# Optimization experiments

Measured on AMD Instinct MI355X. Metric: run time of the kernel, lower is better.

## Reference

```python
import jax, jax.numpy as jnp
import numpy as np
from jax import lax

H, W = 496, 432
NUM_CLASSES = 3
NUM_ROT = 2
A_PER_LOC = NUM_CLASSES * NUM_ROT  # 6
BOX = 7
NMS_PRE = 4096
MAX_NUM = 500
SCORE_THR = 0.1
NMS_THR = 0.5
PI = float(np.pi)


def _make_priors():
    # Anchor3DRangeGenerator equivalent: grid of BEV centers x (3 sizes x 2 rotations)
    xs = jnp.linspace(0.0, 69.12, W, dtype=jnp.float32)
    ys = jnp.linspace(-39.68, 39.68, H, dtype=jnp.float32)
    cy, cx = jnp.meshgrid(ys, xs, indexing='ij')  # [H,W]
    sizes = jnp.array([[3.9, 1.6, 1.56], [0.8, 0.6, 1.73], [1.76, 0.6, 1.73]], jnp.float32)
    szs = jnp.repeat(sizes, NUM_ROT, axis=0)                       # [6,3]
    rots = jnp.tile(jnp.array([0.0, 1.57], jnp.float32), NUM_CLASSES)  # [6]
    cx = jnp.broadcast_to(cx[:, :, None], (H, W, A_PER_LOC))
    cy = jnp.broadcast_to(cy[:, :, None], (H, W, A_PER_LOC))
    cz = jnp.full((H, W, A_PER_LOC), -1.78, jnp.float32)
    wlh = jnp.broadcast_to(szs[None, None], (H, W, A_PER_LOC, 3))
    r = jnp.broadcast_to(rots[None, None], (H, W, A_PER_LOC))
    pri = jnp.concatenate([cx[..., None], cy[..., None], cz[..., None], wlh, r[..., None]], -1)
    return pri.reshape(-1, BOX)  # [H*W*6, 7]


def setup_inputs() -> dict:
    key = jax.random.key(0)
    k1, k2, k3 = jax.random.split(key, 3)
    cls_score = jax.random.normal(k1, (A_PER_LOC * NUM_CLASSES, H, W), jnp.float32)
    bbox_pred = 0.1 * jax.random.normal(k2, (A_PER_LOC * BOX, H, W), jnp.float32)
    dir_cls_pred = jax.random.normal(k3, (A_PER_LOC * 2, H, W), jnp.float32)
    priors = _make_priors()
    return {"cls_score": cls_score, "bbox_pred": bbox_pred,
            "dir_cls_pred": dir_cls_pred, "priors": priors}


def _decode(anchors, deltas):
    xa, ya, za, wa, la, ha, ra = [anchors[:, i] for i in range(7)]
    xt, yt, zt, wt, lt, ht, rt = [deltas[:, i] for i in range(7)]
    za = za + ha / 2
    diag = jnp.sqrt(la ** 2 + wa ** 2)
    xg = xt * diag + xa
    yg = yt * diag + ya
    zg = zt * ha + za
    lg = jnp.exp(lt) * la
    wg = jnp.exp(wt) * wa
    hg = jnp.exp(ht) * ha
    rg = rt + ra
    zg = zg - hg / 2
    return jnp.stack([xg, yg, zg, wg, lg, hg, rg], axis=-1)


def _nms_keep(boxes_xyxy, scores_c, valid_c):
    # Greedy NMS with py_cpu_nms math (+1 pixel convention), fixed-shape masked version.
    n = boxes_xyxy.shape[0]
    order = jnp.argsort(-scores_c)
    b = boxes_xyxy[order]
    v = valid_c[order]
    x1, y1, x2, y2 = b[:, 0], b[:, 1], b[:, 2], b[:, 3]
    areas = (x2 - x1 + 1.0) * (y2 - y1 + 1.0)
    xx1 = jnp.maximum(x1[:, None], x1[None, :])
    yy1 = jnp.maximum(y1[:, None], y1[None, :])
    xx2 = jnp.minimum(x2[:, None], x2[None, :])
    yy2 = jnp.minimum(y2[:, None], y2[None, :])
    inter = jnp.maximum(0.0, xx2 - xx1 + 1.0) * jnp.maximum(0.0, yy2 - yy1 + 1.0)
    iou = inter / (areas[:, None] + areas[None, :] - inter)  # [N,N]
    idx = jnp.arange(n)

    def body(i, keep):
        row = (iou[i] > NMS_THR) & (idx > i)
        return jnp.where(keep[i], keep & ~row, keep)

    keep_sorted = lax.fori_loop(0, n, body, v)
    return jnp.zeros(n, bool).at[order].set(keep_sorted)


def reference(cls_score, bbox_pred, dir_cls_pred, priors):
    # flatten feature maps -> per-anchor predictions
    scores_all = jax.nn.sigmoid(cls_score.transpose(1, 2, 0).reshape(-1, NUM_CLASSES))  # [A,C]
    dir_all = jnp.argmax(dir_cls_pred.transpose(1, 2, 0).reshape(-1, 2), axis=-1)       # [A]
    bp_all = bbox_pred.transpose(1, 2, 0).reshape(-1, BOX)                               # [A,7]
    # nms_pre top-k by best class score
    max_scores = scores_all.max(axis=1)
    _, topk = lax.top_k(max_scores, NMS_PRE)
    pri = priors[topk]
    bp = bp_all[topk]
    sc = scores_all[topk]           # [N,C]
    dsc = dir_all[topk]             # [N]
    bboxes = _decode(pri, bp)       # [N,7] x,y,z,w,l,h,r
    # BEV box -> axis-aligned xyxy (stands in for open3d obb2aabb + xywhr2xyxyr)
    x, y, w, l = bboxes[:, 0], bboxes[:, 1], bboxes[:, 3], bboxes[:, 4]
    boxes_xyxy = jnp.stack([x - w / 2, y - l / 2, x + w / 2, y + l / 2], axis=-1)
    # per-class greedy NMS on the same candidate pool
    valid = sc > SCORE_THR          # [N,C]
    keep = jax.vmap(lambda s, v: _nms_keep(boxes_xyxy, s, v), in_axes=(1, 1))(sc, valid)  # [C,N]
    # merge classes, keep top max_num by score (fixed-shape, padded)
    comb = jnp.where(keep, sc.T, -jnp.inf)                # [C,N]
    top_scores, flat_idx = lax.top_k(comb.reshape(-1), MAX_NUM)
    labels = flat_idx // NMS_PRE
    bidx = flat_idx % NMS_PRE
    sel_b = bboxes[bidx]                                   # [MAX_NUM,7]
    sel_d = dsc[bidx].astype(sel_b.dtype)
    # direction-aware yaw fix (replicates original expression incl. precedence)
    r = sel_b[:, 6]
    dir_rot = r + PI / 2 - jnp.floor(r + 0.5) * PI
    sel_b = sel_b.at[:, 6].set(dir_rot - PI / 2 + PI * sel_d)
    valid_out = jnp.isfinite(top_scores)
    sel_b = jnp.where(valid_out[:, None], sel_b, 0.0)
    out_scores = jnp.where(valid_out, top_scores, 0.0)
    labels = jnp.where(valid_out, labels, -1)
    return sel_b, out_scores, labels
```

## Files before the change

### kernel.cpp

```cpp
#include <hip/hip_runtime.h>
#include <stdint.h>
#include <stddef.h>

constexpr int kH = 496, kW = 432;
constexpr int HWSZ = kH * kW;
constexpr int NANCH = HWSZ * 6;
constexpr int NPRE = 4096;
constexpr int MAXNUM = 500;
constexpr int CAND_CAP = 8192;
constexpr float SCORE_THR_F = 0.1f;
constexpr float PIF  = 3.14159265358979323846f;
constexpr float HPIF = 1.57079632679489661923f;

constexpr int NBINS  = 32768;
constexpr int NPAIR  = NBINS / 2;
constexpr int NB_H   = 256;

constexpr uint64_t PADKEY = 0xFFFFFFFF00000000ull;

constexpr size_t HIST_OFF  = 0;
constexpr size_t MISC_OFF  = 131072;
constexpr size_t ZERO_BYTES= 131072 + 256;
constexpr size_t MS_OFF    = 131328;
constexpr size_t CAND_OFF  = MS_OFF + 4ull * NANCH;
constexpr size_t SEL_OFF   = CAND_OFF + 8ull * CAND_CAP;
constexpr size_t SC3_OFF   = SEL_OFF + 4ull * NPRE;
constexpr size_t DSC_OFF   = SC3_OFF + 4ull * NPRE * 3;
constexpr size_t BB7_OFF   = DSC_OFF + 4ull * NPRE;
constexpr size_t BOX4_OFF  = BB7_OFF + 4ull * NPRE * 7;
constexpr size_t AREA_OFF  = BOX4_OFF + 4ull * NPRE * 4;
constexpr size_t ORD_OFF   = AREA_OFF + 4ull * NPRE;
constexpr size_t VW_OFF    = ORD_OFF + 4ull * 3 * NPRE;
constexpr size_t PMASK_OFF = VW_OFF + 8ull * 3 * 64;
constexpr size_t KEEPW_OFF = PMASK_OFF + 8ull * 3 * NPRE * 64;
constexpr size_t OUTK_OFF  = KEEPW_OFF + 8ull * 3 * 64;

__device__ __forceinline__ float sigmoidf_(float x) { return 1.0f / (1.0f + expf(-x)); }

__device__ __forceinline__ uint64_t readlane64(uint64_t v, int lane) {
  uint32_t lo = (uint32_t)__builtin_amdgcn_readlane((int)(uint32_t)(v & 0xffffffffull), lane);
  uint32_t hi = (uint32_t)__builtin_amdgcn_readlane((int)(uint32_t)(v >> 32), lane);
  return (((uint64_t)hi) << 32) | (uint64_t)lo;
}


__global__ __launch_bounds__(256) void k_score(const float* __restrict__ cls,
                                               float* __restrict__ ms,
                                               uint32_t* __restrict__ hist) {
  __shared__ uint32_t h[NPAIR];
  const int t = threadIdx.x, blk = blockIdx.x;
  for (int i = t; i < NPAIR; i += 256) h[i] = 0;
  __syncthreads();
  for (int p = blk * 256 + t; p < HWSZ; p += NB_H * 256) {
#pragma unroll
    for (int k = 0; k < 6; ++k) {
      float s0 = sigmoidf_(cls[(k * 3 + 0) * HWSZ + p]);
      float s1 = sigmoidf_(cls[(k * 3 + 1) * HWSZ + p]);
      float s2 = sigmoidf_(cls[(k * 3 + 2) * HWSZ + p]);
      float m = fmaxf(s0, fmaxf(s1, s2));
      ms[p * 6 + k] = m;
      uint32_t bin = __float_as_uint(m) >> 15;
      atomicAdd(&h[bin >> 1], 1u << ((bin & 1) * 16));
    }
  }
  __syncthreads();
  for (int i = t; i < NPAIR; i += 256) {
    uint32_t v = h[i];
    if (v) {
      uint32_t lo = v & 0xFFFFu, hi = v >> 16;
      if (lo) atomicAdd(&hist[2 * i],     lo);
      if (hi) atomicAdd(&hist[2 * i + 1], hi);
    }
  }
}

__global__ void k_scanhist(const uint32_t* __restrict__ hist, uint32_t* __restrict__ misc) {
  __shared__ uint32_t part[256];
  __shared__ uint32_t suf[257];
  int t = threadIdx.x;
  int base = t * 128;
  uint32_t s = 0;
  for (int b = 0; b < 128; ++b) s += hist[base + b];
  part[t] = s;
  __syncthreads();
  if (t == 0) {
    uint32_t acc = 0;
    suf[256] = 0;
    for (int q = 255; q >= 0; --q) { suf[q] = acc + part[q]; acc = suf[q]; }
  }
  __syncthreads();
  uint32_t above = suf[t + 1];
  if (above < (uint32_t)NPRE && above + part[t] >= (uint32_t)NPRE) {
    uint32_t acc = above;
    for (int b = base + 127; b >= base; --b) {
      uint32_t h = hist[b];
      if (acc + h >= (uint32_t)NPRE) { misc[1] = (uint32_t)b; misc[2] = acc; break; }
      acc += h;
    }
  }
}

__global__ __launch_bounds__(256) void k_compact(const float* __restrict__ ms,
                                                 uint32_t* __restrict__ misc,
                                                 uint64_t* __restrict__ cand) {
  constexpr int APB = 4096;
  __shared__ uint64_t lbuf[APB];
  __shared__ uint32_t lcnt, lbase;
  const int t = threadIdx.x;
  const int base = blockIdx.x * APB;
  if (t == 0) lcnt = 0;
  __syncthreads();
  const uint32_t B = misc[1];
#pragma unroll
  for (int q = 0; q < 16; ++q) {
    int a = base + q * 256 + t;
    if (a < NANCH) {
      uint32_t bits = __float_as_uint(ms[a]);
      if ((bits >> 15) >= B) {
        uint32_t s = atomicAdd(&lcnt, 1u);
        lbuf[s] = (((uint64_t)(~bits)) << 32) | (uint32_t)a;
      }
    }
  }
  __syncthreads();
  const uint32_t n = lcnt;
  if (t == 0 && n > 0) lbase = atomicAdd(&misc[0], n);
  __syncthreads();
  if (n > 0) {
    const uint32_t b0 = lbase;
    for (uint32_t i = t; i < n; i += 256) {
      uint32_t slot = b0 + i;
      if (slot < (uint32_t)CAND_CAP) cand[slot] = lbuf[i];
    }
  }
}

__global__ __launch_bounds__(256) void k_rank(const uint64_t* __restrict__ cand,
                                              const uint32_t* __restrict__ misc,
                                              uint32_t* __restrict__ sel) {
  const int tid = threadIdx.x, ln = tid & 63;
  const int wave = blockIdx.x * 4 + (tid >> 6);
  const int base = wave * 16;
  uint32_t cnt = misc[0];
  if (cnt > (uint32_t)CAND_CAP) cnt = CAND_CAP;
  uint64_t kr[16];
#pragma unroll
  for (int r = 0; r < 16; ++r) kr[r] = cand[base + r];
  uint32_t rnk[16];
#pragma unroll
  for (int r = 0; r < 16; ++r) rnk[r] = 0;
  const int nch = ((int)cnt + 63) >> 6;
  for (int ch = 0; ch < nch; ++ch) {
    uint64_t ck = cand[ch * 64 + ln];
    uint64_t vm = __ballot(ch * 64 + ln < (int)cnt);
#pragma unroll
    for (int r = 0; r < 16; ++r)
      rnk[r] += (uint32_t)__popcll(__ballot(ck < kr[r]) & vm);
  }
#pragma unroll
  for (int r = 0; r < 16; ++r) {
    int row = base + r;
    if (ln == 0 && row < (int)cnt && rnk[r] < (uint32_t)NPRE)
      sel[rnk[r]] = (uint32_t)kr[r];
  }
}

__global__ void k_gather(const uint32_t* __restrict__ sel, const float* __restrict__ cls,
                         const float* __restrict__ bbp, const float* __restrict__ dirp,
                         const float* __restrict__ priors, float* __restrict__ sc3,
                         uint32_t* __restrict__ dsc, float* __restrict__ bb7,
                         float* __restrict__ box4, float* __restrict__ areaA) {
  int i = blockIdx.x * 256 + threadIdx.x;
  if (i >= NPRE) return;
  uint32_t a = sel[i];
  uint32_t p = a / 6u;
  uint32_t k = a - p * 6u;
#pragma unroll
  for (int c = 0; c < 3; ++c) sc3[i * 3 + c] = sigmoidf_(cls[(k * 3 + c) * HWSZ + p]);
  float d0 = dirp[(k * 2 + 0) * HWSZ + p];
  float d1 = dirp[(k * 2 + 1) * HWSZ + p];
  dsc[i] = (d1 > d0) ? 1u : 0u;
  float dt[7], pr[7];
#pragma unroll
  for (int q = 0; q < 7; ++q) dt[q] = bbp[(k * 7 + q) * HWSZ + p];
#pragma unroll
  for (int q = 0; q < 7; ++q) pr[q] = priors[(size_t)a * 7 + q];
  float za = pr[2] + pr[5] * 0.5f;
  float diag = sqrtf(pr[4] * pr[4] + pr[3] * pr[3]);
  float xg = dt[0] * diag + pr[0];
  float yg = dt[1] * diag + pr[1];
  float zg = dt[2] * pr[5] + za;
  float wg = expf(dt[3]) * pr[3];
  float lg = expf(dt[4]) * pr[4];
  float hg = expf(dt[5]) * pr[5];
  float rg = dt[6] + pr[6];
  zg = zg - hg * 0.5f;
  bb7[i * 7 + 0] = xg; bb7[i * 7 + 1] = yg; bb7[i * 7 + 2] = zg;
  bb7[i * 7 + 3] = wg; bb7[i * 7 + 4] = lg; bb7[i * 7 + 5] = hg; bb7[i * 7 + 6] = rg;
  float x1 = xg - wg * 0.5f, y1 = yg - lg * 0.5f;
  float x2 = xg + wg * 0.5f, y2 = yg + lg * 0.5f;
  box4[i * 4 + 0] = x1; box4[i * 4 + 1] = y1; box4[i * 4 + 2] = x2; box4[i * 4 + 3] = y2;
  areaA[i] = (x2 - x1 + 1.0f) * (y2 - y1 + 1.0f);
}

__global__ __launch_bounds__(256) void k_rankcls(const float* __restrict__ sc3,
                                                 uint32_t* __restrict__ ord) {
  const int tid = threadIdx.x, ln = tid & 63;
  const int c = blockIdx.y;
  const int wave = blockIdx.x * 4 + (tid >> 6);
  const int base = wave * 16;
  uint64_t kr[16];
#pragma unroll
  for (int r = 0; r < 16; ++r) {
    int j = base + r;
    kr[r] = (((uint64_t)(~__float_as_uint(sc3[j * 3 + c]))) << 32) | (uint32_t)j;
  }
  uint32_t rnk[16];
#pragma unroll
  for (int r = 0; r < 16; ++r) rnk[r] = 0;
  for (int ch = 0; ch < NPRE / 64; ++ch) {
    int j = ch * 64 + ln;
    uint64_t ck = (((uint64_t)(~__float_as_uint(sc3[j * 3 + c]))) << 32) | (uint32_t)j;
#pragma unroll
    for (int r = 0; r < 16; ++r)
      rnk[r] += (uint32_t)__popcll(__ballot(ck < kr[r]));
  }
#pragma unroll
  for (int r = 0; r < 16; ++r)
    if (ln == 0) ord[c * NPRE + rnk[r]] = (uint32_t)(base + r);
}

__global__ __launch_bounds__(1024) void k_vwords(const uint32_t* __restrict__ ord,
                                                 const float* __restrict__ sc3,
                                                 uint64_t* __restrict__ vwords) {
  int c = blockIdx.x, t = threadIdx.x, ln = t & 63;
  for (int k = 0; k < 4; ++k) {
    int i = k * 1024 + t;
    uint32_t pos = ord[c * NPRE + i];
    uint64_t m = __ballot(sc3[pos * 3 + c] > SCORE_THR_F);
    if (ln == 0) vwords[c * 64 + (i >> 6)] = m;
  }
}

__global__ void k_mask(const uint32_t* __restrict__ ord, const float* __restrict__ box4,
                       const float* __restrict__ areaA, uint64_t* __restrict__ pmask) {
  int c = blockIdx.z, it = blockIdx.y, jt = blockIdx.x, t = threadIdx.x;
  if (jt < it) return;
  __shared__ float jx1[64], jy1[64], jx2[64], jy2[64], jar[64];
  int j = ord[c * NPRE + jt * 64 + t];
  jx1[t] = box4[j * 4 + 0]; jy1[t] = box4[j * 4 + 1];
  jx2[t] = box4[j * 4 + 2]; jy2[t] = box4[j * 4 + 3];
  jar[t] = areaA[j];
  __syncthreads();
  int I = it * 64 + t;
  int i = ord[c * NPRE + I];
  float x1 = box4[i * 4 + 0], y1 = box4[i * 4 + 1];
  float x2 = box4[i * 4 + 2], y2 = box4[i * 4 + 3];
  float ar = areaA[i];
  uint64_t bits = 0;
  for (int b = 0; b < 64; ++b) {
    float xx1 = fmaxf(x1, jx1[b]), yy1 = fmaxf(y1, jy1[b]);
    float xx2 = fminf(x2, jx2[b]), yy2 = fminf(y2, jy2[b]);
    float iw = fmaxf(0.0f, xx2 - xx1 + 1.0f);
    float ih = fmaxf(0.0f, yy2 - yy1 + 1.0f);
    float inter = iw * ih;
    float iou = inter / (ar + jar[b] - inter);
    bits |= ((uint64_t)(iou > 0.5f)) << b;
  }
  pmask[((size_t)(c * NPRE + I)) * 64 + (size_t)jt] = bits;
}

__global__ __launch_bounds__(320) void k_nms(const uint64_t* __restrict__ pmask,
                                             const uint64_t* __restrict__ vwords,
                                             uint64_t* __restrict__ keepw) {
  __shared__ uint64_t tile[2][64 * 64];
  __shared__ int s_stop[2];
  const int c = blockIdx.x;
  const int tid = threadIdx.x;
  const int wv = tid >> 6;
  const int ln = tid & 63;
  const uint64_t* pm = pmask + (size_t)c * NPRE * 64;

  if (tid == 0) { s_stop[0] = 0; s_stop[1] = 0; }
  if (wv > 0) {
    int l = tid - 64;
    const ulonglong2* src2 = (const ulonglong2*)pm;
    ulonglong2* dst2 = (ulonglong2*)tile[0];
#pragma unroll
    for (int q = 0; q < 8; ++q) dst2[q * 256 + l] = src2[q * 256 + l];
  }
  __syncthreads();

  uint64_t avail = 0, keepbits = 0;
  int cnt = 0;
  if (wv == 0) avail = vwords[c * 64 + ln];

  for (int T = 0; T < 64; ++T) {
    const int cb = T & 1;
    if (wv > 0) {
      if (T + 1 < 64) {
        int l = tid - 64;
        const ulonglong2* src2 = (const ulonglong2*)(pm + (size_t)(T + 1) * 64 * 64);
        ulonglong2* dst2 = (ulonglong2*)tile[cb ^ 1];
#pragma unroll
        for (int q = 0; q < 8; ++q) dst2[q * 256 + l] = src2[q * 256 + l];
      }
    } else {
      const uint64_t* tp = tile[cb];
      uint64_t awT = readlane64(avail, T);
      uint64_t pf[8];
#pragma unroll
      for (int u = 0; u < 8; ++u) pf[u] = tp[u * 64 + ln];
      uint64_t kwT = 0;
#pragma unroll
      for (int r = 0; r < 64; ++r) {
        uint64_t cur = pf[r & 7];
        if (r + 8 < 64) pf[r & 7] = tp[(r + 8) * 64 + ln];
        bool kp = ((awT >> r) & 1ull) != 0ull;
        if (kp) {
          avail &= ~cur;
          awT &= ~readlane64(cur, T);
          kwT |= (1ull << r);
        }
      }
      if (ln == T) keepbits = kwT;
      cnt += (int)__popcll(kwT);
      if (ln == 0 && cnt >= MAXNUM) s_stop[cb] = 1;
    }
    __syncthreads();
    if (s_stop[cb]) break;
  }
  if (wv == 0) keepw[c * 64 + ln] = keepbits;
}

__global__ __launch_bounds__(1024) void k_collect(const uint64_t* __restrict__ keepw,
                                                  const uint32_t* __restrict__ ord,
                                                  const float* __restrict__ sc3,
                                                  uint64_t* __restrict__ outk,
                                                  uint32_t* __restrict__ misc) {
  const int c = blockIdx.x, t = threadIdx.x, w = t >> 6, ln = t & 63;
  if (c == 3) {
    int i = 3 * MAXNUM + t;
    if (i < 2048) outk[i] = PADKEY;
    return;
  }
  __shared__ uint32_t wsum[16];
  uint32_t bits4 = 0;
#pragma unroll
  for (int q = 0; q < 4; ++q) {
    int i = t * 4 + q;
    uint32_t b = (uint32_t)((keepw[c * 64 + (i >> 6)] >> (i & 63)) & 1ull);
    bits4 |= b << q;
  }
  uint32_t cnt = __popc(bits4);
  uint32_t incl = cnt;
#pragma unroll
  for (int d = 1; d < 64; d <<= 1) { uint32_t u = __shfl_up(incl, d, 64); if (ln >= d) incl += u; }
  if (ln == 63) wsum[w] = incl;
  __syncthreads();
  uint32_t wb = 0, total = 0;
#pragma unroll
  for (int i = 0; i < 16; ++i) { uint32_t v = wsum[i]; total += v; if (i < w) wb += v; }
  uint32_t r = wb + incl - cnt;
#pragma unroll
  for (int q = 0; q < 4; ++q) {
    if ((bits4 >> q) & 1u) {
      if (r < (uint32_t)MAXNUM) {
        uint32_t pos = ord[c * NPRE + t * 4 + q];
        uint32_t sb = __float_as_uint(sc3[pos * 3 + c]);
        outk[c * MAXNUM + r] = (((uint64_t)(~sb)) << 32) | (uint32_t)(c * NPRE + pos);
      }
      ++r;
    }
  }
  uint32_t Vc = total < (uint32_t)MAXNUM ? total : (uint32_t)MAXNUM;
  if (t == 0) misc[8 + c] = Vc;
  for (uint32_t s = Vc + t; s < (uint32_t)MAXNUM; s += 1024)
    outk[c * MAXNUM + s] = PADKEY;
}

__global__ __launch_bounds__(256) void k_emit(const uint64_t* __restrict__ outk,
                                              const uint32_t* __restrict__ misc,
                                              const float* __restrict__ bb7,
                                              const uint32_t* __restrict__ dsc,
                                              float* __restrict__ out) {
  const int tid = threadIdx.x, ln = tid & 63;
  const int wave = blockIdx.x * 4 + (tid >> 6);
  const int base = wave * 16;
  uint64_t kr[16];
#pragma unroll
  for (int r = 0; r < 16; ++r) kr[r] = outk[base + r];
  uint32_t rnk[16];
#pragma unroll
  for (int r = 0; r < 16; ++r) rnk[r] = 0;
  for (int ch = 0; ch < 2048 / 64; ++ch) {
    uint64_t ck = outk[ch * 64 + ln];
#pragma unroll
    for (int r = 0; r < 16; ++r)
      rnk[r] += (uint32_t)__popcll(__ballot(ck < kr[r]));
  }
  if (ln == 0) {
#pragma unroll
    for (int r = 0; r < 16; ++r) {
      uint64_t key = kr[r];
      uint32_t rk = rnk[r];
      if (key != PADKEY && rk < (uint32_t)MAXNUM) {
        uint32_t flat = (uint32_t)key;
        float score = __uint_as_float(~((uint32_t)(key >> 32)));
        int cc = (int)(flat >> 12);
        int pos = (int)(flat & 4095u);
        const float* b = bb7 + (size_t)pos * 7;
        float rr0 = b[6];
        float dir_rot = rr0 + HPIF - floorf(rr0 + 0.5f) * PIF;
        float rr = dir_rot - HPIF + PIF * (float)dsc[pos];
#pragma unroll
        for (int q = 0; q < 6; ++q) out[rk * 7 + q] = b[q];
        out[rk * 7 + 6] = rr;
        out[7 * MAXNUM + rk] = score;
        out[8 * MAXNUM + rk] = (float)cc;
      }
    }
  }
  if (blockIdx.x == 0) {
    uint32_t V = misc[8] + misc[9] + misc[10];
    for (uint32_t s = V + tid; s < (uint32_t)MAXNUM; s += 256) {
#pragma unroll
      for (int q = 0; q < 7; ++q) out[s * 7 + q] = 0.0f;
      out[7 * MAXNUM + s] = 0.0f;
      out[8 * MAXNUM + s] = -1.0f;
    }
  }
}

extern "C" void kernel_launch(void* const* d_in, const int* in_sizes, int n_in,
                              void* d_out, int out_size, void* d_ws, size_t ws_size,
                              hipStream_t stream) {
  (void)in_sizes; (void)n_in; (void)out_size; (void)ws_size;
  const float* cls    = (const float*)d_in[0];
  const float* bbp    = (const float*)d_in[1];
  const float* dirp   = (const float*)d_in[2];
  const float* priors = (const float*)d_in[3];
  char* ws = (char*)d_ws;

  uint32_t* hist   = (uint32_t*)(ws + HIST_OFF);
  uint32_t* misc   = (uint32_t*)(ws + MISC_OFF);
  float*    ms     = (float*)(ws + MS_OFF);
  uint64_t* cand   = (uint64_t*)(ws + CAND_OFF);
  uint32_t* sel    = (uint32_t*)(ws + SEL_OFF);
  float*    sc3    = (float*)(ws + SC3_OFF);
  uint32_t* dsc    = (uint32_t*)(ws + DSC_OFF);
  float*    bb7    = (float*)(ws + BB7_OFF);
  float*    box4   = (float*)(ws + BOX4_OFF);
  float*    areaA  = (float*)(ws + AREA_OFF);
  uint32_t* ord    = (uint32_t*)(ws + ORD_OFF);
  uint64_t* vwords = (uint64_t*)(ws + VW_OFF);
  uint64_t* pmask  = (uint64_t*)(ws + PMASK_OFF);
  uint64_t* keepw  = (uint64_t*)(ws + KEEPW_OFF);
  uint64_t* outk   = (uint64_t*)(ws + OUTK_OFF);

  hipMemsetAsync(ws, 0, ZERO_BYTES, stream);
  k_score<<<NB_H, 256, 0, stream>>>(cls, ms, hist);
  k_scanhist<<<1, 256, 0, stream>>>(hist, misc);
  k_compact<<<(NANCH + 4095) / 4096, 256, 0, stream>>>(ms, misc, cand);
  k_rank<<<CAND_CAP / (4 * 16), 256, 0, stream>>>(cand, misc, sel);
  k_gather<<<NPRE / 256, 256, 0, stream>>>(sel, cls, bbp, dirp, priors, sc3, dsc, bb7, box4, areaA);
  k_rankcls<<<dim3(NPRE / (4 * 16), 3), 256, 0, stream>>>(sc3, ord);
  k_vwords<<<3, 1024, 0, stream>>>(ord, sc3, vwords);
  k_mask<<<dim3(64, 64, 3), 64, 0, stream>>>(ord, box4, areaA, pmask);
  k_nms<<<3, 320, 0, stream>>>(pmask, vwords, keepw);
  k_collect<<<4, 1024, 0, stream>>>(keepw, ord, sc3, outk, misc);
  k_emit<<<2048 / (4 * 16), 256, 0, stream>>>(outk, misc, bb7, dsc, (float*)d_out);
}
```

Before: 292.1 us.

## Fold histogram scan into compact and vwords into NMS, make NMS sparse

Removes the single-block histogram scan kernel by having every compact block redundantly scan the histogram with a parallel suffix sum to find the threshold bin. Removes the vwords kernel by computing validity ballots inside the NMS kernel. Rewrites NMS as a single wavefront that iterates only over kept boxes per tile, using ctz loops and direct global reads of diagonal and suppression rows instead of double-buffered shared tiles. This saves launches and serial work, but adds redundant histogram reads in each compact block (about 128 KB per block) and latency-bound global loads in NMS.

```diff
diff --git a/kernel.cpp b/kernel.cpp
--- a/kernel.cpp
+++ b/kernel.cpp
@@ -74,51 +74,59 @@
   }
 }
 
-__global__ void k_scanhist(const uint32_t* __restrict__ hist, uint32_t* __restrict__ misc) {
-  __shared__ uint32_t part[256];
-  __shared__ uint32_t suf[257];
-  int t = threadIdx.x;
-  int base = t * 128;
-  uint32_t s = 0;
-  for (int b = 0; b < 128; ++b) s += hist[base + b];
-  part[t] = s;
-  __syncthreads();
-  if (t == 0) {
-    uint32_t acc = 0;
-    suf[256] = 0;
-    for (int q = 255; q >= 0; --q) { suf[q] = acc + part[q]; acc = suf[q]; }
-  }
-  __syncthreads();
-  uint32_t above = suf[t + 1];
-  if (above < (uint32_t)NPRE && above + part[t] >= (uint32_t)NPRE) {
-    uint32_t acc = above;
-    for (int b = base + 127; b >= base; --b) {
-      uint32_t h = hist[b];
-      if (acc + h >= (uint32_t)NPRE) { misc[1] = (uint32_t)b; misc[2] = acc; break; }
-      acc += h;
-    }
-  }
-}
-
 __global__ __launch_bounds__(256) void k_compact(const float* __restrict__ ms,
+                                                 const uint32_t* __restrict__ hist,
                                                  uint32_t* __restrict__ misc,
                                                  uint64_t* __restrict__ cand) {
   constexpr int APB = 4096;
   __shared__ uint64_t lbuf[APB];
-  __shared__ uint32_t lcnt, lbase;
+  __shared__ uint32_t suf[256];
+  __shared__ uint32_t win[256];
+  __shared__ uint32_t lcnt, lbase, sWin, sAbove, sB;
   const int t = threadIdx.x;
   const int base = blockIdx.x * APB;
-  if (t == 0) lcnt = 0;
-  __syncthreads();
-  const uint32_t B = misc[1];
+
+  uint32_t s = 0;
+  const int hbase = t * 128;
+#pragma unroll 16
+  for (int i = 0; i < 128; ++i) s += hist[hbase + i];
+  suf[t] = s;
+  if (t == 0) { lcnt = 0; sB = 0; }
+  __syncthreads();
+  for (int d = 1; d < 256; d <<= 1) {
+    uint32_t v = suf[t] + ((t + d < 256) ? suf[t + d] : 0u);
+    __syncthreads();
+    suf[t] = v;
+    __syncthreads();
+  }
+  {
+    uint32_t sin = suf[t];
+    uint32_t sup = (t < 255) ? suf[t + 1] : 0u;
+    if (sin >= (uint32_t)NPRE && sup < (uint32_t)NPRE) { sWin = (uint32_t)t; sAbove = sup; }
+  }
+  __syncthreads();
+  const uint32_t wbase = sWin * 128u;
+  win[t] = (t < 128) ? hist[wbase + (uint32_t)t] : 0u;
+  __syncthreads();
+  for (int d = 1; d < 256; d <<= 1) {
+    uint32_t v = win[t] + ((t + d < 256) ? win[t + d] : 0u);
+    __syncthreads();
+    win[t] = v;
+    __syncthreads();
+  }
+  if (t < 128 && sAbove + win[t] >= (uint32_t)NPRE)
+    atomicMax(&sB, wbase + (uint32_t)t);
+  __syncthreads();
+  const uint32_t B = sB;
+
 #pragma unroll
   for (int q = 0; q < 16; ++q) {
     int a = base + q * 256 + t;
     if (a < NANCH) {
       uint32_t bits = __float_as_uint(ms[a]);
       if ((bits >> 15) >= B) {
-        uint32_t s = atomicAdd(&lcnt, 1u);
-        lbuf[s] = (((uint64_t)(~bits)) << 32) | (uint32_t)a;
+        uint32_t sl = atomicAdd(&lcnt, 1u);
+        lbuf[sl] = (((uint64_t)(~bits)) << 32) | (uint32_t)a;
       }
     }
   }
@@ -230,18 +238,6 @@
     if (ln == 0) ord[c * NPRE + rnk[r]] = (uint32_t)(base + r);
 }
 
-__global__ __launch_bounds__(1024) void k_vwords(const uint32_t* __restrict__ ord,
-                                                 const float* __restrict__ sc3,
-                                                 uint64_t* __restrict__ vwords) {
-  int c = blockIdx.x, t = threadIdx.x, ln = t & 63;
-  for (int k = 0; k < 4; ++k) {
-    int i = k * 1024 + t;
-    uint32_t pos = ord[c * NPRE + i];
-    uint64_t m = __ballot(sc3[pos * 3 + c] > SCORE_THR_F);
-    if (ln == 0) vwords[c * 64 + (i >> 6)] = m;
-  }
-}
-
 __global__ void k_mask(const uint32_t* __restrict__ ord, const float* __restrict__ box4,
                        const float* __restrict__ areaA, uint64_t* __restrict__ pmask) {
   int c = blockIdx.z, it = blockIdx.y, jt = blockIdx.x, t = threadIdx.x;
@@ -270,67 +266,63 @@
   pmask[((size_t)(c * NPRE + I)) * 64 + (size_t)jt] = bits;
 }
 
-__global__ __launch_bounds__(320) void k_nms(const uint64_t* __restrict__ pmask,
-                                             const uint64_t* __restrict__ vwords,
-                                             uint64_t* __restrict__ keepw) {
-  __shared__ uint64_t tile[2][64 * 64];
-  __shared__ int s_stop[2];
+__global__ __launch_bounds__(64) void k_nms(const uint64_t* __restrict__ pmask,
+                                            const uint32_t* __restrict__ ord,
+                                            const float* __restrict__ sc3,
+                                            uint64_t* __restrict__ keepw) {
   const int c = blockIdx.x;
-  const int tid = threadIdx.x;
-  const int wv = tid >> 6;
-  const int ln = tid & 63;
+  const int ln = threadIdx.x;
   const uint64_t* pm = pmask + (size_t)c * NPRE * 64;
 
-  if (tid == 0) { s_stop[0] = 0; s_stop[1] = 0; }
-  if (wv > 0) {
-    int l = tid - 64;
-    const ulonglong2* src2 = (const ulonglong2*)pm;
-    ulonglong2* dst2 = (ulonglong2*)tile[0];
-#pragma unroll
-    for (int q = 0; q < 8; ++q) dst2[q * 256 + l] = src2[q * 256 + l];
-  }
-  __syncthreads();
-
-  uint64_t avail = 0, keepbits = 0;
+  uint64_t avail = 0;
+  for (int w = 0; w < 64; w += 4) {
+    uint32_t p0 = ord[c * NPRE + (w + 0) * 64 + ln];
+    uint32_t p1 = ord[c * NPRE + (w + 1) * 64 + ln];
+    uint32_t p2 = ord[c * NPRE + (w + 2) * 64 + ln];
+    uint32_t p3 = ord[c * NPRE + (w + 3) * 64 + ln];
+    uint64_t m0 = __ballot(sc3[p0 * 3 + c] > SCORE_THR_F);
+    uint64_t m1 = __ballot(sc3[p1 * 3 + c] > SCORE_THR_F);
+    uint64_t m2 = __ballot(sc3[p2 * 3 + c] > SCORE_THR_F);
+    uint64_t m3 = __ballot(sc3[p3 * 3 + c] > SCORE_THR_F);
+    if (ln == w + 0) avail = m0;
+    if (ln == w + 1) avail = m1;
+    if (ln == w + 2) avail = m2;
+    if (ln == w + 3) avail = m3;
+  }
+
+  uint64_t dg_cur = pm[((size_t)(0 * 64 + ln)) * 64 + 0];
+  uint64_t dg_nxt = pm[((size_t)(1 * 64 + ln)) * 64 + 1];
+
+  uint64_t mykeep = 0;
   int cnt = 0;
-  if (wv == 0) avail = vwords[c * 64 + ln];
-
   for (int T = 0; T < 64; ++T) {
-    const int cb = T & 1;
-    if (wv > 0) {
-      if (T + 1 < 64) {
-        int l = tid - 64;
-        const ulonglong2* src2 = (const ulonglong2*)(pm + (size_t)(T + 1) * 64 * 64);
-        ulonglong2* dst2 = (ulonglong2*)tile[cb ^ 1];
-#pragma unroll
-        for (int q = 0; q < 8; ++q) dst2[q * 256 + l] = src2[q * 256 + l];
+    const int Tp = (T + 2 <= 63) ? (T + 2) : 63;
+    uint64_t dg_n2 = pm[((size_t)(Tp * 64 + ln)) * 64 + (size_t)Tp];
+
+    uint64_t awT = readlane64(avail, T);
+    uint64_t kwT = 0;
+    while (awT) {
+      int r = (int)__builtin_ctzll(awT);
+      kwT |= (1ull << r);
+      awT &= ~(1ull << r);
+      awT &= ~readlane64(dg_cur, r);
+    }
+    if (kwT) {
+      uint64_t supp = 0, k = kwT;
+      while (k) {
+        int r = (int)__builtin_ctzll(k);
+        k &= k - 1;
+        supp |= pm[((size_t)(T * 64 + r)) * 64 + (size_t)ln];
       }
-    } else {
-      const uint64_t* tp = tile[cb];
-      uint64_t awT = readlane64(avail, T);
-      uint64_t pf[8];
-#pragma unroll
-      for (int u = 0; u < 8; ++u) pf[u] = tp[u * 64 + ln];
-      uint64_t kwT = 0;
-#pragma unroll
-      for (int r = 0; r < 64; ++r) {
-        uint64_t cur = pf[r & 7];
-        if (r + 8 < 64) pf[r & 7] = tp[(r + 8) * 64 + ln];
-        bool kp = ((awT >> r) & 1ull) != 0ull;
-        if (kp) {
-          avail &= ~cur;
-          awT &= ~readlane64(cur, T);
-          kwT |= (1ull << r);
-        }
-      }
-      if (ln == T) keepbits = kwT;
+      avail &= ~supp;
+      if (ln == T) mykeep = kwT;
       cnt += (int)__popcll(kwT);
-      if (ln == 0 && cnt >= MAXNUM) s_stop[cb] = 1;
-    }
-    __syncthreads();
-    if (s_stop[cb]) break;
-  }
-  if (wv == 0) keepw[c * 64 + ln] = keepbits;
+      if (cnt >= MAXNUM) break;
+    }
+    dg_cur = dg_nxt;
+    dg_nxt = dg_n2;
+  }
+  keepw[c * 64 + ln] = mykeep;
 }
 
 __global__ __launch_bounds__(1024) void k_collect(const uint64_t* __restrict__ keepw,
@@ -453,21 +445,18 @@
   float*    box4   = (float*)(ws + BOX4_OFF);
   float*    areaA  = (float*)(ws + AREA_OFF);
   uint32_t* ord    = (uint32_t*)(ws + ORD_OFF);
-  uint64_t* vwords = (uint64_t*)(ws + VW_OFF);
   uint64_t* pmask  = (uint64_t*)(ws + PMASK_OFF);
   uint64_t* keepw  = (uint64_t*)(ws + KEEPW_OFF);
   uint64_t* outk   = (uint64_t*)(ws + OUTK_OFF);
 
   hipMemsetAsync(ws, 0, ZERO_BYTES, stream);
   k_score<<<NB_H, 256, 0, stream>>>(cls, ms, hist);
-  k_scanhist<<<1, 256, 0, stream>>>(hist, misc);
-  k_compact<<<(NANCH + 4095) / 4096, 256, 0, stream>>>(ms, misc, cand);
+  k_compact<<<(NANCH + 4095) / 4096, 256, 0, stream>>>(ms, hist, misc, cand);
   k_rank<<<CAND_CAP / (4 * 16), 256, 0, stream>>>(cand, misc, sel);
   k_gather<<<NPRE / 256, 256, 0, stream>>>(sel, cls, bbp, dirp, priors, sc3, dsc, bb7, box4, areaA);
   k_rankcls<<<dim3(NPRE / (4 * 16), 3), 256, 0, stream>>>(sc3, ord);
-  k_vwords<<<3, 1024, 0, stream>>>(ord, sc3, vwords);
   k_mask<<<dim3(64, 64, 3), 64, 0, stream>>>(ord, box4, areaA, pmask);
-  k_nms<<<3, 320, 0, stream>>>(pmask, vwords, keepw);
+  k_nms<<<3, 64, 0, stream>>>(pmask, ord, sc3, keepw);
   k_collect<<<4, 1024, 0, stream>>>(keepw, ord, sc3, outk, misc);
   k_emit<<<2048 / (4 * 16), 256, 0, stream>>>(outk, misc, bb7, dsc, (float*)d_out);
 }
```

New measurement: 432.2 us. 48.0% more time.
